# Kernel tuning notes

Hardware: AMD Instinct MI355X
Metric: run time of the kernel (lower is better)

## Reference

```python
import jax, jax.numpy as jnp
import numpy as np

B, T, D, H, HD = 128, 256, 512, 8, 64

def setup_inputs() -> dict:
    key = jax.random.key(0)
    ks = jax.random.split(key, 5)
    scale = 0.02
    return {
        "x": jax.random.normal(ks[0], (B, T, D), dtype=jnp.float32),
        "Wq": jax.random.normal(ks[1], (H, D, HD), dtype=jnp.float32) * scale,
        "Wk": jax.random.normal(ks[2], (H, D, HD), dtype=jnp.float32) * scale,
        "Wv": jax.random.normal(ks[3], (H, D, HD), dtype=jnp.float32) * scale,
        "Wo": jax.random.normal(ks[4], (D, D), dtype=jnp.float32) * scale,
        "bo": jnp.zeros((D,), dtype=jnp.float32),
    }

def reference(x, Wq, Wk, Wv, Wo, bo):
    # Per-head projections, batched over heads: [B,T,D] x [H,D,HD] -> [B,H,T,HD]
    q = jnp.einsum('btd,hdk->bhtk', x, Wq)
    k = jnp.einsum('btd,hdk->bhtk', x, Wk)
    v = jnp.einsum('btd,hdk->bhtk', x, Wv)
    # Scaled scores [B,H,T,T] with causal mask
    scores = jnp.einsum('bhtk,bhsk->bhts', q, k) * (HD ** -0.5)
    causal = jnp.tril(jnp.ones((T, T), dtype=bool))
    scores = jnp.where(causal, scores, jnp.finfo(scores.dtype).min)
    attn = jax.nn.softmax(scores, axis=-1)
    # Dropout is identity at inference.
    out = jnp.einsum('bhts,bhsk->bhtk', attn, v)
    # Concat heads: [B,T,H*HD] == [B,T,D]
    out = out.transpose(0, 2, 1, 3).reshape(B, T, D)
    # Output projection
    return out @ Wo + bo
```

## Files before the change

### kernel.cpp

```cpp
#include <hip/hip_runtime.h>
#include <hip/hip_bf16.h>

typedef __bf16 bf16x8 __attribute__((ext_vector_type(8)));
typedef __bf16 bf16x4 __attribute__((ext_vector_type(4)));
typedef float f32x4 __attribute__((ext_vector_type(4)));
typedef unsigned short u16x8 __attribute__((ext_vector_type(8)));


__device__ __forceinline__ unsigned short f2bf(float f) {
  unsigned u = __float_as_uint(f);
  u += 0x7fffu + ((u >> 16) & 1u);
  return (unsigned short)(u >> 16);
}

__device__ __forceinline__ bf16x4 cvt4(f32x4 v) {
  bf16x4 o;
  o[0] = (__bf16)v[0]; o[1] = (__bf16)v[1]; o[2] = (__bf16)v[2]; o[3] = (__bf16)v[3];
  return o;
}

__device__ __forceinline__ void async16(const void* g, void* l) {
  __builtin_amdgcn_global_load_lds(
      (const __attribute__((address_space(1))) void*)g,
      (__attribute__((address_space(3))) void*)l, 16, 0, 0);
}

__global__ __launch_bounds__(256) void k_convert_x(const float* __restrict__ in,
                                                   unsigned short* __restrict__ out) {
  int i = blockIdx.x * 256 + threadIdx.x;
  const float4* p = (const float4*)in + (size_t)i * 2;
  float4 a = p[0], b = p[1];
  u16x8 o;
  o[0] = f2bf(a.x); o[1] = f2bf(a.y); o[2] = f2bf(a.z); o[3] = f2bf(a.w);
  o[4] = f2bf(b.x); o[5] = f2bf(b.y); o[6] = f2bf(b.z); o[7] = f2bf(b.w);
  *((u16x8*)out + i) = o;
}

__global__ __launch_bounds__(256) void k_transpose_w3(const float* __restrict__ w0,
                                                      const float* __restrict__ w1,
                                                      const float* __restrict__ w2,
                                                      unsigned short* __restrict__ out) {
  __shared__ unsigned short tile[64][72];
  int z = blockIdx.z;
  int wsel = z >> 3, hsel = z & 7;
  const float* inb = (wsel == 0 ? w0 : (wsel == 1 ? w1 : w2)) + (size_t)hsel * 512 * 64;
  unsigned short* outb = out + (size_t)z * 512 * 64;
  int r0 = blockIdx.y * 64;
  int tid = threadIdx.x;
  int r = tid >> 2, cq = (tid & 3) * 16;
  const float* src = inb + (size_t)(r0 + r) * 64 + cq;
#pragma unroll
  for (int i = 0; i < 16; i += 4) {
    float4 v = *(const float4*)(src + i);
    tile[r][cq + i + 0] = f2bf(v.x);
    tile[r][cq + i + 1] = f2bf(v.y);
    tile[r][cq + i + 2] = f2bf(v.z);
    tile[r][cq + i + 3] = f2bf(v.w);
  }
  __syncthreads();
  int cr = tid >> 2, rq = (tid & 3) * 16;
  u16x8 o0, o1;
#pragma unroll
  for (int i = 0; i < 8; ++i) o0[i] = tile[rq + i][cr];
#pragma unroll
  for (int i = 0; i < 8; ++i) o1[i] = tile[rq + 8 + i][cr];
  unsigned short* dst = outb + (size_t)cr * 512 + r0 + rq;
  *(u16x8*)dst = o0;
  *(u16x8*)(dst + 8) = o1;
}

__global__ __launch_bounds__(256) void k_transpose_w(const float* __restrict__ in,
                                                     unsigned short* __restrict__ out,
                                                     int rows, int cols) {
  __shared__ unsigned short tile[64][72];
  int c0 = blockIdx.x * 64, r0 = blockIdx.y * 64;
  int tid = threadIdx.x;
  int r = tid >> 2, cq = (tid & 3) * 16;
  const float* src = in + (size_t)(r0 + r) * cols + c0 + cq;
#pragma unroll
  for (int i = 0; i < 16; i += 4) {
    float4 v = *(const float4*)(src + i);
    tile[r][cq + i + 0] = f2bf(v.x);
    tile[r][cq + i + 1] = f2bf(v.y);
    tile[r][cq + i + 2] = f2bf(v.z);
    tile[r][cq + i + 3] = f2bf(v.w);
  }
  __syncthreads();
  int cr = tid >> 2, rq = (tid & 3) * 16;
  u16x8 o0, o1;
#pragma unroll
  for (int i = 0; i < 8; ++i) o0[i] = tile[rq + i][cr];
#pragma unroll
  for (int i = 0; i < 8; ++i) o1[i] = tile[rq + 8 + i][cr];
  unsigned short* dst = out + (size_t)(c0 + cr) * rows + r0 + rq;
  *(u16x8*)dst = o0;
  *(u16x8*)(dst + 8) = o1;
}

template <int KIND>
__global__ __launch_bounds__(512, 1) void k_gemmP(
    const unsigned short* __restrict__ A,
    const unsigned short* __restrict__ Bmat,
    unsigned short* __restrict__ O0,
    unsigned short* __restrict__ O1,
    const float* __restrict__ bo,
    float* __restrict__ outf) {
  __shared__ unsigned short smem[65536];
  const int P = (KIND == 0) ? 64 : 32;
  int xcd = blockIdx.x & 7, g = blockIdx.x >> 3;
  int w = xcd * P + g;
  int mt, nt;
  if (KIND == 0) { mt = w >> 2; nt = w & 3; }
  else           { mt = w >> 1; nt = w & 1; }
  int m0 = mt * 256, n0 = nt * 256;
  int tid = threadIdx.x;
  int wid = tid >> 6, lane = tid & 63;
  int lr = lane & 15, lg = lane >> 4;
  int wm = wid >> 2, wn = wid & 3;

  int srow_off = wid * 16 + (lane >> 3);
  int schunk = (lane & 7) ^ (lane >> 3);
  auto stageA = [&](int kb, int buf, int half) {
#pragma unroll
    for (int j = 0; j < 2; ++j) {
      int row = half * 128 + srow_off + j * 8;
      async16(A + (size_t)(m0 + row) * 512 + kb * 64 + schunk * 8,
              smem + buf * 32768 + half * 8192 + (wid * 2 + j) * 512);
    }
  };
  auto stageB = [&](int kb, int buf, int half) {
#pragma unroll
    for (int j = 0; j < 2; ++j) {
      int row = half * 128 + srow_off + j * 8;
      async16(Bmat + (size_t)(n0 + row) * 512 + kb * 64 + schunk * 8,
              smem + buf * 32768 + 16384 + half * 8192 + (wid * 2 + j) * 512);
    }
  };
  auto lda = [&](int buf, int mi, int k32) -> bf16x8 {
    int row = mi * 32 + wm * 16 + lr;
    int ch = (k32 * 4 + lg) ^ (lr & 7);
    return *(const bf16x8*)&smem[buf * 32768 + row * 64 + ch * 8];
  };
  auto ldb = [&](int buf, int ni, int k32) -> bf16x8 {
    int row = ni * 64 + wn * 16 + lr;
    int ch = (k32 * 4 + lg) ^ (lr & 7);
    return *(const bf16x8*)&smem[buf * 32768 + 16384 + row * 64 + ch * 8];
  };

  f32x4 acc[8][4];
#pragma unroll
  for (int mi = 0; mi < 8; ++mi)
#pragma unroll
    for (int ni = 0; ni < 4; ++ni) acc[mi][ni] = (f32x4){0.f, 0.f, 0.f, 0.f};

#define MF(dst, afrag, bfrag)                                                        \
  if constexpr (KIND == 2)                                                           \
    dst = __builtin_amdgcn_mfma_f32_16x16x32_bf16(afrag, bfrag, dst, 0, 0, 0);       \
  else                                                                               \
    dst = __builtin_amdgcn_mfma_f32_16x16x32_bf16(bfrag, afrag, dst, 0, 0, 0);

  stageA(0, 0, 0); stageB(0, 0, 0); stageA(0, 0, 1); stageB(0, 0, 1);
  asm volatile("s_waitcnt vmcnt(4)" ::: "memory");
  __builtin_amdgcn_s_barrier();
  asm volatile("" ::: "memory");

  bf16x8 a03[4][2], a47[4][2], b01[2][2], b23[2][2];
#pragma unroll
  for (int t = 0; t < 8; ++t) {
    int buf = t & 1, nbuf = buf ^ 1;
    const bool st = (t < 7);
#pragma unroll
    for (int mi = 0; mi < 4; ++mi) { a03[mi][0] = lda(buf, mi, 0); a03[mi][1] = lda(buf, mi, 1); }
#pragma unroll
    for (int ni = 0; ni < 2; ++ni) { b01[ni][0] = ldb(buf, ni, 0); b01[ni][1] = ldb(buf, ni, 1); }
    if (st) stageA(t + 1, nbuf, 0);
    asm volatile("" ::: "memory");
    __builtin_amdgcn_s_setprio(1);
#pragma unroll
    for (int mi = 0; mi < 4; ++mi)
#pragma unroll
      for (int ni = 0; ni < 2; ++ni)
#pragma unroll
        for (int k = 0; k < 2; ++k) { MF(acc[mi][ni], a03[mi][k], b01[ni][k]); }
    __builtin_amdgcn_s_setprio(0);
    if (st) asm volatile("s_waitcnt vmcnt(4)" ::: "memory");
    else    asm volatile("s_waitcnt vmcnt(2)" ::: "memory");
    __builtin_amdgcn_s_barrier();
    asm volatile("" ::: "memory");
#pragma unroll
    for (int mi = 0; mi < 4; ++mi) { a47[mi][0] = lda(buf, mi + 4, 0); a47[mi][1] = lda(buf, mi + 4, 1); }
    if (st) stageB(t + 1, nbuf, 0);
    asm volatile("" ::: "memory");
    __builtin_amdgcn_s_setprio(1);
#pragma unroll
    for (int mi = 0; mi < 4; ++mi)
#pragma unroll
      for (int ni = 0; ni < 2; ++ni)
#pragma unroll
        for (int k = 0; k < 2; ++k) { MF(acc[mi + 4][ni], a47[mi][k], b01[ni][k]); }
    __builtin_amdgcn_s_setprio(0);
    if (st) asm volatile("s_waitcnt vmcnt(4)" ::: "memory");
    else    asm volatile("s_waitcnt vmcnt(0)" ::: "memory");
    __builtin_amdgcn_s_barrier();
    asm volatile("" ::: "memory");
#pragma unroll
    for (int ni = 0; ni < 2; ++ni) { b23[ni][0] = ldb(buf, ni + 2, 0); b23[ni][1] = ldb(buf, ni + 2, 1); }
    if (st) stageA(t + 1, nbuf, 1);
    asm volatile("" ::: "memory");
    __builtin_amdgcn_s_setprio(1);
#pragma unroll
    for (int mi = 0; mi < 4; ++mi)
#pragma unroll
      for (int ni = 0; ni < 2; ++ni)
#pragma unroll
        for (int k = 0; k < 2; ++k) { MF(acc[mi + 4][ni + 2], a47[mi][k], b23[ni][k]); }
    __builtin_amdgcn_s_setprio(0);
    __builtin_amdgcn_s_barrier();
    asm volatile("" ::: "memory");
    if (st) stageB(t + 1, nbuf, 1);
    asm volatile("" ::: "memory");
    __builtin_amdgcn_s_setprio(1);
#pragma unroll
    for (int mi = 0; mi < 4; ++mi)
#pragma unroll
      for (int ni = 0; ni < 2; ++ni)
#pragma unroll
        for (int k = 0; k < 2; ++k) { MF(acc[mi][ni + 2], a03[mi][k], b23[ni][k]); }
    __builtin_amdgcn_s_setprio(0);
    if (st) asm volatile("s_waitcnt vmcnt(4)" ::: "memory");
    __builtin_amdgcn_s_barrier();
    asm volatile("" ::: "memory");
  }
#undef MF

  if constexpr (KIND == 0) {
    int z = n0 >> 9;
    if (z == 0) {
#pragma unroll
      for (int mi = 0; mi < 8; ++mi)
#pragma unroll
        for (int ni = 0; ni < 4; ++ni) acc[mi][ni] *= 0.18033688011112042f;
    }
    int hbase = (n0 & 511) >> 6;
    int hd0 = wn * 16 + lg * 4;
#pragma unroll
    for (int ni = 0; ni < 4; ++ni) {
      unsigned short* outp = (z ? O1 : O0) + (size_t)(mt * 8 + hbase + ni) * 16384;
#pragma unroll
      for (int mi = 0; mi < 8; ++mi) {
        int tq = mi * 32 + wm * 16 + lr;
        *(bf16x4*)&outp[(size_t)tq * 64 + hd0] = cvt4(acc[mi][ni]);
      }
    }
  } else if constexpr (KIND == 1) {
#pragma unroll
    for (int ni = 0; ni < 4; ++ni) {
      int nb = n0 + ni * 64 + wn * 16 + lg * 4;
      float4 b4 = *(const float4*)&bo[nb];
#pragma unroll
      for (int mi = 0; mi < 8; ++mi) {
        int mg = m0 + mi * 32 + wm * 16 + lr;
        float4 o;
        o.x = acc[mi][ni][0] + b4.x; o.y = acc[mi][ni][1] + b4.y;
        o.z = acc[mi][ni][2] + b4.z; o.w = acc[mi][ni][3] + b4.w;
        *(float4*)&outf[(size_t)mg * 512 + nb] = o;
      }
    }
  } else {
    int hbase = n0 >> 6;
    int hd = wn * 16 + lr;
#pragma unroll
    for (int ni = 0; ni < 4; ++ni) {
      unsigned short* outp = O0 + (size_t)(mt * 8 + hbase + ni) * 16384;
#pragma unroll
      for (int mi = 0; mi < 8; ++mi) {
        int tq = mi * 32 + wm * 16 + lg * 4;
        *(bf16x4*)&outp[(size_t)hd * 256 + tq] = cvt4(acc[mi][ni]);
      }
    }
  }
}

__global__ __launch_bounds__(512, 4) void k_attn2(
    const unsigned short* __restrict__ Qb,
    const unsigned short* __restrict__ Kb,
    const unsigned short* __restrict__ Vtb,
    unsigned short* __restrict__ Ob) {
  __shared__ unsigned short Ks[16384];
  __shared__ unsigned short Vs[16384];
  __shared__ unsigned short Ps[8][16][36];
  int bh = blockIdx.x;
  int tid = threadIdx.x, wid = tid >> 6, lane = tid & 63, lr = lane & 15, lg = lane >> 4;
  int bb = bh >> 3, h = bh & 7;
  const unsigned short* Kg = Kb + (size_t)bh * 16384;
  const unsigned short* Vg = Vtb + (size_t)bh * 16384;
#pragma unroll
  for (int c = 0; c < 4; ++c) {
    int d = (wid * 4 + c) * 64 + lane;
    int kr = d >> 3, kc = (d & 7) ^ (kr & 7);
    async16(Kg + (size_t)kr * 64 + kc * 8, Ks + (wid * 4 + c) * 512);
  }
  int ci0 = wid, ci1 = 15 - wid;
  const unsigned short* q0 = Qb + (size_t)bh * 16384 + (size_t)(ci0 * 16 + lr) * 64 + lg * 8;
  const unsigned short* q1 = Qb + (size_t)bh * 16384 + (size_t)(ci1 * 16 + lr) * 64 + lg * 8;
  bf16x8 bq0a = *(const bf16x8*)q0;
  bf16x8 bq0b = *(const bf16x8*)(q0 + 32);
  bf16x8 bq1a = *(const bf16x8*)q1;
  bf16x8 bq1b = *(const bf16x8*)(q1 + 32);
#pragma unroll
  for (int c = 0; c < 4; ++c) {
    int d = (wid * 4 + c) * 64 + lane;
    int vr = d >> 5, vc = (d & 31) ^ ((vr & 7) << 2);
    async16(Vg + (size_t)vr * 256 + vc * 8, Vs + (wid * 4 + c) * 512);
  }
  asm volatile("s_waitcnt vmcnt(4)" ::: "memory");
  __builtin_amdgcn_s_barrier();
  asm volatile("" ::: "memory");

  auto do_chunk = [&](int ci, bf16x8 bqa, bf16x8 bqb, bool waitV) {
    int t0 = ci * 16, trow = t0 + lr;
    int ntV = ci + 1;
    int ntE = (ntV + 1) & ~1;
    int nk32 = ntE >> 1;
    f32x4 acc[16];
#pragma unroll
    for (int nt = 0; nt < 16; ++nt)
      if (nt < ntV) {
        acc[nt] = (f32x4){0.f, 0.f, 0.f, 0.f};
        int row = nt * 16 + lr;
        bf16x8 ak0 = *(const bf16x8*)&Ks[row * 64 + ((0 + lg) ^ (lr & 7)) * 8];
        acc[nt] = __builtin_amdgcn_mfma_f32_16x16x32_bf16(ak0, bqa, acc[nt], 0, 0, 0);
        bf16x8 ak1 = *(const bf16x8*)&Ks[row * 64 + ((4 + lg) ^ (lr & 7)) * 8];
        acc[nt] = __builtin_amdgcn_mfma_f32_16x16x32_bf16(ak1, bqb, acc[nt], 0, 0, 0);
      }
    float m = -3.0e38f;
#pragma unroll
    for (int nt = 0; nt < 16; ++nt)
      if (nt < ntV) {
        if (nt == ci) {
#pragma unroll
          for (int r = 0; r < 4; ++r) {
            float v = acc[nt][r];
            if (lg * 4 + r > lr) v = -1.0e30f;
            acc[nt][r] = v;
            m = fmaxf(m, v);
          }
        } else {
#pragma unroll
          for (int r = 0; r < 4; ++r) m = fmaxf(m, acc[nt][r]);
        }
      }
    m = fmaxf(m, __shfl_xor(m, 16));
    m = fmaxf(m, __shfl_xor(m, 32));
    float s4[4] = {0.f, 0.f, 0.f, 0.f};
    bf16x4 pk[16];
#pragma unroll
    for (int nt = 0; nt < 16; ++nt)
      if (nt < ntV) {
#pragma unroll
        for (int r = 0; r < 4; ++r) {
          float p = exp2f(acc[nt][r] - m);
          s4[r] += p;
          pk[nt][r] = (__bf16)p;
        }
      }
    if (ntV & 1) {
      pk[ntV][0] = (__bf16)0.f; pk[ntV][1] = (__bf16)0.f;
      pk[ntV][2] = (__bf16)0.f; pk[ntV][3] = (__bf16)0.f;
    }
    float s = (s4[0] + s4[1]) + (s4[2] + s4[3]);
    s += __shfl_xor(s, 16);
    s += __shfl_xor(s, 32);
    float inv = 1.0f / s;
    if (waitV) {
      asm volatile("s_waitcnt vmcnt(0)" ::: "memory");
      __builtin_amdgcn_s_barrier();
      asm volatile("" ::: "memory");
    }
    *(bf16x4*)&Ps[wid][lr][lg * 4] = pk[0];
    *(bf16x4*)&Ps[wid][lr][16 + lg * 4] = pk[1];
    f32x4 aco[4];
#pragma unroll
    for (int vt = 0; vt < 4; ++vt) aco[vt] = (f32x4){0.f, 0.f, 0.f, 0.f};
#pragma unroll
    for (int k32 = 0; k32 < 8; ++k32)
      if (k32 < nk32) {
        bf16x8 pb = *(const bf16x8*)&Ps[wid][lr][lg * 8];
        if (k32 + 1 < nk32) {
          *(bf16x4*)&Ps[wid][lr][lg * 4] = pk[2 * k32 + 2];
          *(bf16x4*)&Ps[wid][lr][16 + lg * 4] = pk[2 * k32 + 3];
        }
#pragma unroll
        for (int vt = 0; vt < 4; ++vt) {
          int row = vt * 16 + lr;
          bf16x8 av = *(const bf16x8*)&Vs[row * 256 + (((k32 * 4 + lg) ^ ((lr & 7) << 2)) * 8)];
          aco[vt] = __builtin_amdgcn_mfma_f32_16x16x32_bf16(av, pb, aco[vt], 0, 0, 0);
        }
      }
    unsigned short* obase = Ob + (size_t)(bb * 256 + trow) * 512 + h * 64 + lg * 4;
#pragma unroll
    for (int vt = 0; vt < 4; ++vt) {
      bf16x4 ov;
#pragma unroll
      for (int r = 0; r < 4; ++r) ov[r] = (__bf16)(aco[vt][r] * inv);
      *(bf16x4*)(obase + vt * 16) = ov;
    }
  };

  do_chunk(ci0, bq0a, bq0b, true);
  do_chunk(ci1, bq1a, bq1b, false);
}

extern "C" void kernel_launch(void* const* d_in, const int* in_sizes, int n_in,
                              void* d_out, int out_size, void* d_ws, size_t ws_size,
                              hipStream_t stream) {
  (void)in_sizes; (void)n_in; (void)out_size; (void)ws_size;
  const float* x = (const float*)d_in[0];
  const float* Wq = (const float*)d_in[1];
  const float* Wk = (const float*)d_in[2];
  const float* Wv = (const float*)d_in[3];
  const float* Wo = (const float*)d_in[4];
  const float* bo = (const float*)d_in[5];
  float* out = (float*)d_out;
  char* ws = (char*)d_ws;
  const size_t MB = 1024 * 1024;
  unsigned short* Qb = (unsigned short*)(ws);
  unsigned short* Kb = (unsigned short*)(ws + 32 * MB);
  unsigned short* Vtb = (unsigned short*)(ws + 64 * MB);
  unsigned short* xb = (unsigned short*)(ws + 96 * MB);
  unsigned short* Wqt = (unsigned short*)(ws + 128 * MB);
  unsigned short* Wkt = Wqt + 262144;
  unsigned short* Wvt = Wkt + 262144;
  unsigned short* Wot = Wvt + 262144;

  hipLaunchKernelGGL(k_convert_x, dim3(8192), dim3(256), 0, stream, x, xb);
  hipLaunchKernelGGL(k_transpose_w3, dim3(1, 8, 24), dim3(256), 0, stream, Wq, Wk, Wv, Wqt);
  hipLaunchKernelGGL(k_transpose_w, dim3(8, 8, 1), dim3(256), 0, stream, Wo, Wot, 512, 512);
  hipLaunchKernelGGL((k_gemmP<0>), dim3(512), dim3(512), 0, stream,
                     xb, Wqt, Qb, Kb, (const float*)nullptr, (float*)nullptr);
  hipLaunchKernelGGL((k_gemmP<2>), dim3(256), dim3(512), 0, stream,
                     xb, Wvt, Vtb, (unsigned short*)nullptr, (const float*)nullptr, (float*)nullptr);
  hipLaunchKernelGGL(k_attn2, dim3(1024), dim3(512), 0, stream, Qb, Kb, Vtb, xb);
  hipLaunchKernelGGL((k_gemmP<1>), dim3(256), dim3(512), 0, stream,
                     xb, Wot, (unsigned short*)nullptr, (unsigned short*)nullptr, bo, out);
}
```

Before: 169.3 us.

## Stage K/V through registers into padded LDS layout instead of async swizzled loads

Replaces the async global-to-LDS loads with XOR-swizzled addressing by register loads followed by stores into a padded (stride 34) split LDS layout for K and V. LDS fragment reads then use precomputed base pointers plus constant offsets, which removes the per-access swizzle arithmetic. The split wait for V that overlapped its load with the QK/softmax phase is gone; a single __syncthreads now waits for both K and V. The row max also uses two partial accumulators. This trades the previous load/compute overlap and the direct-to-LDS path for simpler addressing and a conflict-avoiding padded layout, at the cost of extra register staging and slightly more LDS.

```diff
diff --git a/kernel.cpp b/kernel.cpp
--- a/kernel.cpp
+++ b/kernel.cpp
@@ -286,19 +286,21 @@
     const unsigned short* __restrict__ Kb,
     const unsigned short* __restrict__ Vtb,
     unsigned short* __restrict__ Ob) {
-  __shared__ unsigned short Ks[16384];
-  __shared__ unsigned short Vs[16384];
+  __shared__ unsigned short Ksh[2 * 256 * 34];
+  __shared__ unsigned short Vsh[8 * 64 * 34];
   __shared__ unsigned short Ps[8][16][36];
   int bh = blockIdx.x;
   int tid = threadIdx.x, wid = tid >> 6, lane = tid & 63, lr = lane & 15, lg = lane >> 4;
   int bb = bh >> 3, h = bh & 7;
   const unsigned short* Kg = Kb + (size_t)bh * 16384;
   const unsigned short* Vg = Vtb + (size_t)bh * 16384;
-#pragma unroll
-  for (int c = 0; c < 4; ++c) {
-    int d = (wid * 4 + c) * 64 + lane;
-    int kr = d >> 3, kc = (d & 7) ^ (kr & 7);
-    async16(Kg + (size_t)kr * 64 + kc * 8, Ks + (wid * 4 + c) * 512);
+  int4 gk[4], gv[4];
+#pragma unroll
+  for (int j = 0; j < 4; ++j) {
+    int ck = tid * 4 + j;
+    gk[j] = *(const int4*)(Kg + (ck >> 3) * 64 + (ck & 7) * 8);
+    int cv = tid * 4 + j;
+    gv[j] = *(const int4*)(Vg + (cv >> 5) * 256 + (cv & 31) * 8);
   }
   int ci0 = wid, ci1 = 15 - wid;
   const unsigned short* q0 = Qb + (size_t)bh * 16384 + (size_t)(ci0 * 16 + lr) * 64 + lg * 8;
@@ -308,32 +310,35 @@
   bf16x8 bq1a = *(const bf16x8*)q1;
   bf16x8 bq1b = *(const bf16x8*)(q1 + 32);
 #pragma unroll
-  for (int c = 0; c < 4; ++c) {
-    int d = (wid * 4 + c) * 64 + lane;
-    int vr = d >> 5, vc = (d & 31) ^ ((vr & 7) << 2);
-    async16(Vg + (size_t)vr * 256 + vc * 8, Vs + (wid * 4 + c) * 512);
-  }
-  asm volatile("s_waitcnt vmcnt(4)" ::: "memory");
-  __builtin_amdgcn_s_barrier();
-  asm volatile("" ::: "memory");
-
-  auto do_chunk = [&](int ci, bf16x8 bqa, bf16x8 bqb, bool waitV) {
+  for (int j = 0; j < 4; ++j) {
+    int ck = tid * 4 + j;
+    int rr = ck >> 3, o = ck & 7;
+    *(int4*)&Ksh[(o >> 2) * 8704 + rr * 34 + (o & 3) * 8] = gk[j];
+    int cv = tid * 4 + j;
+    int vr = cv >> 5, vo = cv & 31;
+    *(int4*)&Vsh[(vo >> 2) * 2176 + vr * 34 + (vo & 3) * 8] = gv[j];
+  }
+  __syncthreads();
+
+  const unsigned short* kbase = &Ksh[lr * 34 + lg * 8];
+  const unsigned short* vbase = &Vsh[lr * 34 + lg * 8];
+  unsigned short* psw = &Ps[wid][lr][0];
+
+  auto do_chunk = [&](int ci, bf16x8 bqa, bf16x8 bqb) {
     int t0 = ci * 16, trow = t0 + lr;
     int ntV = ci + 1;
-    int ntE = (ntV + 1) & ~1;
-    int nk32 = ntE >> 1;
+    int nk32 = (ntV + 1) >> 1;
     f32x4 acc[16];
 #pragma unroll
     for (int nt = 0; nt < 16; ++nt)
       if (nt < ntV) {
         acc[nt] = (f32x4){0.f, 0.f, 0.f, 0.f};
-        int row = nt * 16 + lr;
-        bf16x8 ak0 = *(const bf16x8*)&Ks[row * 64 + ((0 + lg) ^ (lr & 7)) * 8];
+        bf16x8 ak0 = *(const bf16x8*)(kbase + nt * 544);
         acc[nt] = __builtin_amdgcn_mfma_f32_16x16x32_bf16(ak0, bqa, acc[nt], 0, 0, 0);
-        bf16x8 ak1 = *(const bf16x8*)&Ks[row * 64 + ((4 + lg) ^ (lr & 7)) * 8];
+        bf16x8 ak1 = *(const bf16x8*)(kbase + nt * 544 + 8704);
         acc[nt] = __builtin_amdgcn_mfma_f32_16x16x32_bf16(ak1, bqb, acc[nt], 0, 0, 0);
       }
-    float m = -3.0e38f;
+    float m0c = -3.0e38f, m1c = -3.0e38f;
 #pragma unroll
     for (int nt = 0; nt < 16; ++nt)
       if (nt < ntV) {
@@ -343,13 +348,12 @@
             float v = acc[nt][r];
             if (lg * 4 + r > lr) v = -1.0e30f;
             acc[nt][r] = v;
-            m = fmaxf(m, v);
           }
-        } else {
-#pragma unroll
-          for (int r = 0; r < 4; ++r) m = fmaxf(m, acc[nt][r]);
         }
-      }
+        m0c = fmaxf(m0c, fmaxf(acc[nt][0], acc[nt][1]));
+        m1c = fmaxf(m1c, fmaxf(acc[nt][2], acc[nt][3]));
+      }
+    float m = fmaxf(m0c, m1c);
     m = fmaxf(m, __shfl_xor(m, 16));
     m = fmaxf(m, __shfl_xor(m, 32));
     float s4[4] = {0.f, 0.f, 0.f, 0.f};
@@ -372,28 +376,22 @@
     s += __shfl_xor(s, 16);
     s += __shfl_xor(s, 32);
     float inv = 1.0f / s;
-    if (waitV) {
-      asm volatile("s_waitcnt vmcnt(0)" ::: "memory");
-      __builtin_amdgcn_s_barrier();
-      asm volatile("" ::: "memory");
-    }
-    *(bf16x4*)&Ps[wid][lr][lg * 4] = pk[0];
-    *(bf16x4*)&Ps[wid][lr][16 + lg * 4] = pk[1];
+    *(bf16x4*)(psw + lg * 4) = pk[0];
+    *(bf16x4*)(psw + 16 + lg * 4) = pk[1];
     f32x4 aco[4];
 #pragma unroll
     for (int vt = 0; vt < 4; ++vt) aco[vt] = (f32x4){0.f, 0.f, 0.f, 0.f};
 #pragma unroll
-    for (int k32 = 0; k32 < 8; ++k32)
-      if (k32 < nk32) {
-        bf16x8 pb = *(const bf16x8*)&Ps[wid][lr][lg * 8];
-        if (k32 + 1 < nk32) {
-          *(bf16x4*)&Ps[wid][lr][lg * 4] = pk[2 * k32 + 2];
-          *(bf16x4*)&Ps[wid][lr][16 + lg * 4] = pk[2 * k32 + 3];
+    for (int kk = 0; kk < 8; ++kk)
+      if (kk < nk32) {
+        bf16x8 pb = *(const bf16x8*)(psw + lg * 8);
+        if (kk + 1 < nk32) {
+          *(bf16x4*)(psw + lg * 4) = pk[2 * kk + 2];
+          *(bf16x4*)(psw + 16 + lg * 4) = pk[2 * kk + 3];
         }
 #pragma unroll
         for (int vt = 0; vt < 4; ++vt) {
-          int row = vt * 16 + lr;
-          bf16x8 av = *(const bf16x8*)&Vs[row * 256 + (((k32 * 4 + lg) ^ ((lr & 7) << 2)) * 8)];
+          bf16x8 av = *(const bf16x8*)(vbase + kk * 2176 + vt * 544);
           aco[vt] = __builtin_amdgcn_mfma_f32_16x16x32_bf16(av, pb, aco[vt], 0, 0, 0);
         }
       }
@@ -407,8 +405,8 @@
     }
   };
 
-  do_chunk(ci0, bq0a, bq0b, true);
-  do_chunk(ci1, bq1a, bq1b, false);
+  do_chunk(ci0, bq0a, bq0b);
+  do_chunk(ci1, bq1a, bq1b);
 }
 
 extern "C" void kernel_launch(void* const* d_in, const int* in_sizes, int n_in,
```

After: 204.6 us. 1.21x slower.
